# Kernel tuning notes

Hardware: AMD Instinct MI355X
Metric: run time of the kernel (lower is better)

The kernel has to match this reference:

```python
import jax, jax.numpy as jnp
import numpy as np

# Dimensions (production-scale, see shape_source)
B, L, D = 16, 64, 256      # batch, text length, char_emb
U = 500                    # number of distinct units (characters/phonemes)
V = 10000                  # vocab size
MIN_WL, MAX_WL = 4, 10     # min/max extracted word length
WL = MAX_WL - MIN_WL + 1   # number of candidate word lengths (7)
TEMP = 0.1                 # g.temperature
INS_COST = 1.0             # per-character insertion/deletion cost


def setup_inputs() -> dict:
    key = jax.random.key(0)
    k1, k2, k3, k4 = jax.random.split(key, 4)
    word_repr = jax.random.normal(k1, (B, L, D), jnp.float32)
    unit_repr = jax.random.normal(k2, (U, D), jnp.float32)
    indexed_segments = jax.random.randint(k3, (V, MAX_WL), 0, U)
    vocab_length = jax.random.randint(k4, (V,), MIN_WL, MAX_WL + 1)
    return {
        "word_repr": word_repr,
        "unit_repr": unit_repr,
        "indexed_segments": indexed_segments,
        "vocab_length": vocab_length,
    }


def _soft_max(x, axis):
    w = jnp.exp(jax.nn.log_softmax(x / TEMP, axis=axis))
    value = (x * w).sum(axis)
    index = jnp.argmax(x, axis=axis)
    return value, index


def _soft_min(x, axis):
    w = jnp.exp(jax.nn.log_softmax(-x / TEMP, axis=axis))
    value = (x * w).sum(axis)
    index = jnp.argmin(x, axis=axis)
    return value, index


def _soft_threshold(x):
    return (jax.nn.celu(1.0 - 2.0 * x) + 1.0) / 2.0


def reference(word_repr, unit_repr, indexed_segments, vocab_length):
    # --- cosine char-similarity between text positions and vocab units ---
    wn = word_repr / jnp.linalg.norm(word_repr, axis=-1, keepdims=True)   # (B,L,D)
    un = unit_repr / jnp.linalg.norm(unit_repr, axis=-1, keepdims=True)   # (U,D)
    sim = jnp.einsum('bld,ud->blu', wn, un)                               # (B,L,U)
    # pad along length so s+j gathers are in-range; padded dist is masked later
    simp = jnp.pad(sim, ((0, 0), (0, MAX_WL), (0, 0)))                    # (B,L+ML,U)

    wls = jnp.arange(MIN_WL, MAX_WL + 1)                                  # (WL,)

    # --- aligned edit-distance accumulation d(v, w) over char positions ---
    # ed[b,s,k,v] = sum_{j < min(wl_k, len_v)} (1 - cos(text[b,s+j], vocab_char[v,j]))
    ed = jnp.zeros((B, L, WL, V), jnp.float32)
    for j in range(MAX_WL):
        d_j = 1.0 - simp[:, j:j + L, :][:, :, indexed_segments[:, j]]     # (B,L,V)
        m_j = (j < jnp.minimum(wls[:, None], vocab_length[None, :]))      # (WL,V)
        ed = ed + d_j[:, :, None, :] * m_j.astype(jnp.float32)[None, None]
    # length-mismatch penalty (insert/delete)
    ed = ed + INS_COST * jnp.abs(wls[:, None] - vocab_length[None, :]).astype(jnp.float32)

    # --- soft-min over vocab: matched_ed_dist / matched_vocab ---
    matched_ed, matched_vocab = _soft_min(ed, axis=-1)                    # (B,L,WL)
    matched_length = vocab_length[matched_vocab]                          # (B,L,WL)
    # soft threshold on per-character distance, then score = thresh * |w|
    matched_thresh = _soft_threshold(matched_ed / wls.astype(jnp.float32))
    matched_score = matched_thresh * wls.astype(jnp.float32)              # (B,L,WL)

    # --- viability and scatter restore into dense (batch, len_s, len_e) ---
    s_idx = jnp.arange(L)[:, None]                                        # (L,1)
    viable = (s_idx + wls[None, :]) <= L                                  # (L,WL)
    score = jnp.where(viable[None], matched_score, 0.0)                   # (B,L,WL)
    e_idx = jnp.clip(s_idx + wls[None, :] - 1, 0, L - 1)                  # (L,WL)
    s_grid = jnp.broadcast_to(s_idx, (L, WL))
    dense = jnp.zeros((B, L, L), jnp.float32).at[:, s_grid, e_idx].add(
        score * viable[None].astype(jnp.float32))                         # (B,len_s,len_e)

    # --- soft-max over all candidate spans ---
    flat = dense.reshape(B, L * L)
    best_score, best_idx = _soft_max(flat, axis=-1)                       # (B,)
    start = best_idx // L
    end = best_idx % L
    wl_sel = jnp.clip(end - start + 1 - MIN_WL, 0, WL - 1)
    best_vocab = matched_vocab[jnp.arange(B), start, wl_sel]              # (B,)

    return start, end, best_score, best_vocab, dense
```

## Files before the change

kernel.cpp:

```cpp
#include <hip/hip_runtime.h>

#define NB 16
#define NL 64
#define ND 256
#define NU 500
#define NV 10000
#define MINWL 4
#define MAXWL 10
#define NWL 7
#define ITEMP 10.0f
#define L2I 14.4269504088896f
#define NT 512
#define NTX 1024
#define NWAVES 16
#define NCH 16
#define RSTR 501
#define DLPAD 32568
#define SEGL_SLOTS 648
#define EXT_LDS_BYTES ((DLPAD + SEGL_SLOTS * 8) * 4)
#define NSK (NWL * 64)
#define NZERO 3690.0f

__global__ __launch_bounds__(512) void k_sort(const int* __restrict__ vlen,
                                              int* __restrict__ origv,
                                              int* __restrict__ bases) {
    int t = threadIdx.x;
    const int CH = 20;
    int lo = t * CH, hi = min(lo + CH, NV);
    unsigned long long hA = 0, hB = 0;
    for (int v = lo; v < hi; ++v) {
        int l = vlen[v] - MINWL;
        int sh = (l & 3) * 16;
        unsigned long long inc = 1ULL << sh;
        bool isA = l < 4;
        hA += isA ? inc : 0ULL;
        hB += isA ? 0ULL : inc;
    }
    int lane = t & 63, wv = t >> 6;
    unsigned long long iA = hA, iB = hB;
#pragma unroll
    for (int o = 1; o < 64; o <<= 1) {
        unsigned long long a2 = (unsigned long long)__shfl_up((long long)iA, o);
        unsigned long long b2 = (unsigned long long)__shfl_up((long long)iB, o);
        if (lane >= o) { iA += a2; iB += b2; }
    }
    __shared__ unsigned long long wA[8], wB[8];
    __shared__ int base_s[8];
    if (lane == 63) { wA[wv] = iA; wB[wv] = iB; }
    __syncthreads();
    unsigned long long pA = 0, pB = 0, tA = 0, tB = 0;
#pragma unroll
    for (int w2 = 0; w2 < 8; ++w2) {
        if (w2 < wv) { pA += wA[w2]; pB += wB[w2]; }
        tA += wA[w2]; tB += wB[w2];
    }
    unsigned long long eA = pA + iA - hA, eB = pB + iB - hB;
    if (t == 0) {
        int tot[7] = {(int)(tA & 0xFFFF), (int)((tA >> 16) & 0xFFFF),
                      (int)((tA >> 32) & 0xFFFF), (int)((tA >> 48) & 0xFFFF),
                      (int)(tB & 0xFFFF), (int)((tB >> 16) & 0xFFFF),
                      (int)((tB >> 32) & 0xFFFF)};
        int run = 0;
        for (int l = 0; l < 7; ++l) { base_s[l] = run; bases[l] = run; run += tot[l]; }
        base_s[7] = run; bases[7] = run;
    }
    __syncthreads();
    unsigned long long qA = eA + ((unsigned long long)base_s[0] |
                                  ((unsigned long long)base_s[1] << 16) |
                                  ((unsigned long long)base_s[2] << 32) |
                                  ((unsigned long long)base_s[3] << 48));
    unsigned long long qB = eB + ((unsigned long long)base_s[4] |
                                  ((unsigned long long)base_s[5] << 16) |
                                  ((unsigned long long)base_s[6] << 32));
    for (int v = lo; v < hi; ++v) {
        int l = vlen[v] - MINWL;
        int sh = (l & 3) * 16;
        bool isA = l < 4;
        unsigned long long cur = isA ? qA : qB;
        int pos = (int)((cur >> sh) & 0xFFFF);
        origv[pos] = v;
        unsigned long long inc = 1ULL << sh;
        qA += isA ? inc : 0ULL;
        qB += isA ? 0ULL : inc;
    }
}

__global__ __launch_bounds__(256) void k_gather(const int* __restrict__ origv,
                                                const int* __restrict__ seg,
                                                unsigned int* __restrict__ segP) {
    int i = blockIdx.x * 256 + threadIdx.x;
    if (i >= NV) return;
    int v = origv[i];
    const int2* sp = (const int2*)(seg + v * MAXWL);
    int2 a0 = sp[0], a1 = sp[1], a2 = sp[2], a3 = sp[3], a4 = sp[4];
    unsigned int* dst = segP + i * 8;
    *(uint4*)dst = make_uint4((unsigned)(a0.x | (a0.y << 16)),
                              (unsigned)(a1.x | (a1.y << 16)),
                              (unsigned)(a2.x | (a2.y << 16)),
                              (unsigned)(a3.x | (a3.y << 16)));
    dst[4] = (unsigned)(a4.x | (a4.y << 16));
}

#define SSTR 260
#define SIM_LDS_BYTES ((2 * 32 * SSTR + 64) * 4)

__global__ __launch_bounds__(256) void k_sim(const float* __restrict__ word,
                                             const float* __restrict__ unit,
                                             float* __restrict__ sim) {
    extern __shared__ float lds[];
    float* wt = lds;
    float* ut = lds + 32 * SSTR;
    float* scaleW = lds + 64 * SSTR;
    float* scaleU = scaleW + 32;
    int blk = blockIdx.x;
    int uc = blk & 15, lt = (blk >> 4) & 1, b = blk >> 5;
    int l0 = lt * 32, u0 = uc * 32;
    int t = threadIdx.x;

#pragma unroll
    for (int i = 0; i < 32; ++i)
        wt[i * SSTR + t] = word[(b * NL + l0 + i) * ND + t];
#pragma unroll
    for (int i = 0; i < 32; ++i) {
        int u = u0 + i;
        ut[i * SSTR + t] = (u < NU) ? unit[u * ND + t] : 1.0f;
    }
    __syncthreads();
#pragma unroll
    for (int h = 0; h < 2; ++h) {
        int r = (t >> 4) + h * 16, p = t & 15;
        float sw = 0.f, su = 0.f;
#pragma unroll
        for (int c = 0; c < 16; ++c) {
            float x = wt[r * SSTR + p * 16 + c];
            float y = ut[r * SSTR + p * 16 + c];
            sw += x * x; su += y * y;
        }
#pragma unroll
        for (int o = 1; o < 16; o <<= 1) {
            sw += __shfl_xor(sw, o);
            su += __shfl_xor(su, o);
        }
        if (p == 0) { scaleW[r] = 1.0f / sqrtf(sw); scaleU[r] = 1.0f / sqrtf(su); }
    }
    __syncthreads();

    int lane = t & 15;
    int lp = t >> 4;
    int l = lp * 2;
    const float4* w0p = (const float4*)(wt + l * SSTR);
    const float4* w1p = (const float4*)(wt + (l + 1) * SSTR);
    const float4* x0p = (const float4*)(ut + lane * SSTR);
    const float4* x1p = (const float4*)(ut + (lane + 16) * SSTR);
    float a00 = 0.f, a01 = 0.f, a10 = 0.f, a11 = 0.f;
#pragma unroll 8
    for (int dq = 0; dq < ND / 4; ++dq) {
        float4 w0 = w0p[dq], w1 = w1p[dq], x0 = x0p[dq], x1 = x1p[dq];
        a00 += w0.x * x0.x + w0.y * x0.y + w0.z * x0.z + w0.w * x0.w;
        a01 += w0.x * x1.x + w0.y * x1.y + w0.z * x1.z + w0.w * x1.w;
        a10 += w1.x * x0.x + w1.y * x0.y + w1.z * x0.z + w1.w * x0.w;
        a11 += w1.x * x1.x + w1.y * x1.y + w1.z * x1.z + w1.w * x1.w;
    }
    float sw0 = scaleW[l], sw1 = scaleW[l + 1];
    float su0 = scaleU[lane], su1 = scaleU[lane + 16];
    int gu0 = u0 + lane, gu1 = u0 + lane + 16;
    int base = (b * NL + l0 + l) * NU;
    if (gu0 < NU) { sim[base + gu0] = a00 * (sw0 * su0); sim[base + NU + gu0] = a10 * (sw1 * su0); }
    if (gu1 < NU) { sim[base + gu1] = a01 * (sw0 * su1); sim[base + NU + gu1] = a11 * (sw1 * su1); }
}


template <int L>
__device__ __forceinline__ void item_one(const unsigned int* __restrict__ segL,
                                         int li, const float* __restrict__ dl,
                                         const int* __restrict__ rowoff,
                                         float& Sb, float& Wb, float& mb, int& ixb,
                                         float& Sm, float& Wm, float& mmv, int& ixm) {
    const unsigned int* sp = segL + li * 8;
    uint4 p = *(const uint4*)sp;
    unsigned int w4 = (L > 8) ? sp[4] : 0u;
    unsigned int c[10];
    c[0] = p.x & 0xFFFF; c[1] = p.x >> 16;
    c[2] = p.y & 0xFFFF; c[3] = p.y >> 16;
    c[4] = p.z & 0xFFFF; c[5] = p.z >> 16;
    c[6] = p.w & 0xFFFF; c[7] = p.w >> 16;
    c[8] = w4 & 0xFFFF;  c[9] = w4 >> 16;
    float q = ((dl[rowoff[0] + c[0]] + dl[rowoff[1] + c[1]]) +
               dl[rowoff[2] + c[2]]) + dl[rowoff[3] + c[3]];
    float pm = q;
#pragma unroll
    for (int j = 4; j < L; ++j) {
        if (j == L - 1) pm = q;
        q += dl[rowoff[j] + c[j]];
    }
    float wb = __builtin_amdgcn_exp2f(fmaf(q, -L2I, (float)L * L2I));
    Sb += wb;
    Wb = fmaf(q, wb, Wb);
    bool lb = q < mb;
    ixb = lb ? li : ixb;
    mb = lb ? q : mb;
    if constexpr (L >= 5) {
        float edm = pm + 1.0f;
        float wm = __builtin_amdgcn_exp2f(fmaf(edm, -L2I, (float)(L - 1) * L2I));
        Sm += wm;
        Wm = fmaf(edm, wm, Wm);
        bool lm = edm < mmv;
        ixm = lm ? li : ixm;
        mmv = lm ? edm : mmv;
    }
}

template <int L>
__device__ __forceinline__ void bucket_passL(int a, int e, int gofs,
                                             const unsigned int* __restrict__ segL,
                                             const float* __restrict__ dl,
                                             const int* __restrict__ rowoff,
                                             float* m, float* S, float* W, int* ix) {
    if (a >= e) return;
    float Sb = 0.f, Wb = 0.f, mb = 3.0e38f;
    float Sm = 0.f, Wm = 0.f, mmv = 3.0e38f;
    int ixb = 0, ixm = 0;
    int li = a;
    for (; li + 1 < e; li += 2) {
        item_one<L>(segL, li, dl, rowoff, Sb, Wb, mb, ixb, Sm, Wm, mmv, ixm);
        item_one<L>(segL, li + 1, dl, rowoff, Sb, Wb, mb, ixb, Sm, Wm, mmv, ixm);
    }
    if (li < e)
        item_one<L>(segL, li, dl, rowoff, Sb, Wb, mb, ixb, Sm, Wm, mmv, ixm);

    int gb = ixb + gofs, gm_ = ixm + gofs;
#pragma unroll
    for (int k = 0; k < NWL; ++k) {
        if (k >= L - 4) {
            float c = (float)(k + 4 - L);
            S[k] += Sb;
            W[k] += fmaf(c, Sb, Wb);
            float cand = mb + c;
            bool take = (cand < m[k]) || (cand == m[k] && gb < ix[k]);
            ix[k] = take ? gb : ix[k];
            m[k] = take ? cand : m[k];
        }
        if constexpr (L >= 5) {
            if (k == L - 5) {
                S[k] += Sm;
                W[k] += Wm;
                bool take = (mmv < m[k]) || (mmv == m[k] && gm_ < ix[k]);
                ix[k] = take ? gm_ : ix[k];
                m[k] = take ? mmv : m[k];
            }
        }
    }
}

__global__ __launch_bounds__(NTX, 1) void k_extract(const float* __restrict__ sim,
                                                    const unsigned int* __restrict__ segP,
                                                    const int* __restrict__ basesG,
                                                    float* __restrict__ pM,
                                                    float* __restrict__ pS,
                                                    float* __restrict__ pW,
                                                    int* __restrict__ pI) {
    extern __shared__ float dl[];
    unsigned int* segL = (unsigned int*)(dl + DLPAD);
    int blk = blockIdx.x;
    int ch = blk & (NCH - 1), b = blk >> 4;
    int t = threadIdx.x;
    int s = t & 63, w = t >> 6;

    int cs[7], ne[7], lb[7];
    {
        int run = 0;
#pragma unroll
        for (int l = 0; l < 7; ++l) {
            int lo = basesG[l], hi = basesG[l + 1];
            int n = hi - lo;
            int pc = (n + NCH - 1) >> 4;
            int c0 = lo + ch * pc;
            int c1 = min(c0 + pc, hi);
            cs[l] = c0;
            ne[l] = max(c1 - c0, 0);
            lb[l] = run;
            run += ne[l];
        }
    }

    {
        const float2* simq = (const float2*)(sim + b * NL * NU);
        for (int idx = t; idx < NL * 250; idx += NTX) {
            int r = idx / 250;
            int u2 = idx - r * 250;
            float2 g = simq[idx];
            float* ds = dl + r * RSTR + u2 * 2;
            ds[0] = 1.0f - g.x;
            ds[1] = 1.0f - g.y;
        }
        if (t < NU + 1) dl[64 * RSTR + t] = 0.0f;
    }
#pragma unroll
    for (int l = 0; l < 7; ++l) {
        for (int ii = t; ii < ne[l]; ii += NTX) {
            const unsigned int* gp = segP + (cs[l] + ii) * 8;
            uint4 pv = *(const uint4*)gp;
            unsigned int w4 = gp[4];
            unsigned int* dp = segL + (lb[l] + ii) * 8;
            *(uint4*)dp = pv;
            dp[4] = w4;
        }
    }
    __syncthreads();

    int rowoff[10];
#pragma unroll
    for (int j = 0; j < 10; ++j) rowoff[j] = min(s + j, 64) * RSTR;

    float m[NWL], S[NWL], W[NWL];
    int ix[NWL];
#pragma unroll
    for (int k = 0; k < NWL; ++k) { m[k] = 3.0e38f; S[k] = 0.f; W[k] = 0.f; ix[k] = 0; }

    int la[7], le[7];
#pragma unroll
    for (int l = 0; l < 7; ++l) {
        int pw = (ne[l] + NWAVES - 1) >> 4;
        la[l] = lb[l] + w * pw;
        le[l] = min(la[l] + pw, lb[l] + ne[l]);
    }
    bucket_passL<4>(la[0], le[0], cs[0] - lb[0], segL, dl, rowoff, m, S, W, ix);
    bucket_passL<5>(la[1], le[1], cs[1] - lb[1], segL, dl, rowoff, m, S, W, ix);
    bucket_passL<6>(la[2], le[2], cs[2] - lb[2], segL, dl, rowoff, m, S, W, ix);
    bucket_passL<7>(la[3], le[3], cs[3] - lb[3], segL, dl, rowoff, m, S, W, ix);
    bucket_passL<8>(la[4], le[4], cs[4] - lb[4], segL, dl, rowoff, m, S, W, ix);
    bucket_passL<9>(la[5], le[5], cs[5] - lb[5], segL, dl, rowoff, m, S, W, ix);
    bucket_passL<10>(la[6], le[6], cs[6] - lb[6], segL, dl, rowoff, m, S, W, ix);

    __syncthreads();
    float* scrM = dl;
    float* scrS = dl + NWAVES * NSK;
    float* scrW = dl + 2 * NWAVES * NSK;
    int* scrI = (int*)(dl + 3 * NWAVES * NSK);
#pragma unroll
    for (int k = 0; k < NWL; ++k) {
        int o = (w * NWL + k) * 64 + s;
        scrM[o] = m[k]; scrS[o] = S[k]; scrW[o] = W[k]; scrI[o] = ix[k];
    }
    __syncthreads();
    if (t < NSK) {
        int k = t >> 6, ss = t & 63;
        int o0 = k * 64 + ss;
        float mm = scrM[o0], SS = scrS[o0], WW = scrW[o0];
        int II = scrI[o0];
#pragma unroll
        for (int w2 = 1; w2 < NWAVES; ++w2) {
            int o = (w2 * NWL + k) * 64 + ss;
            float m2 = scrM[o];
            int i2 = scrI[o];
            bool take = (m2 < mm) || (m2 == mm && i2 < II);
            II = take ? i2 : II;
            mm = take ? m2 : mm;
            SS += scrS[o];
            WW += scrW[o];
        }
        int off = (b * NCH + ch) * NSK + t;
        pM[off] = mm; pS[off] = SS; pW[off] = WW; pI[off] = II;
    }
}

__global__ __launch_bounds__(NT) void k_merge(const float* __restrict__ pM,
                                              const float* __restrict__ pS,
                                              const float* __restrict__ pW,
                                              const int* __restrict__ pI,
                                              const int* __restrict__ origv,
                                              float* __restrict__ out) {
    int b = blockIdx.x, t = threadIdx.x;
    __shared__ float score[NSK];
    __shared__ int ixf[NSK];
    __shared__ float rm[8], rS[8], rW[8];
    __shared__ int rX[8];
    __shared__ float gm;
    __shared__ int gfl;

    float x = -1.0f;
    int fl = 0x7FFFFFFF;
    if (t < NSK) {
        int base = b * NCH * NSK + t;
        float mm = pM[base], SS = pS[base], WW = pW[base];
        int II = pI[base];
        for (int c = 1; c < NCH; ++c) {
            int o = base + c * NSK;
            float m2 = pM[o];
            int i2 = pI[o];
            bool take = (m2 < mm) || (m2 == mm && i2 < II);
            II = take ? i2 : II;
            mm = take ? m2 : mm;
            SS += pS[o];
            WW += pW[o];
        }
        int k = t >> 6, ss = t & 63;
        int kmax = min(NWL - 1, 60 - ss);
        if (k <= kmax) {
            float med = WW / SS;
            float wl = (float)(MINWL + k);
            float z = 1.0f - 2.0f * (med / wl);
            float cel = (z > 0.f) ? z : (__expf(z) - 1.0f);
            x = 0.5f * (cel + 1.0f) * wl;
            ixf[t] = II;
            fl = ss * 64 + (ss + k + 3);
        }
        score[t] = (k <= kmax) ? x : 0.0f;
    }
    __syncthreads();

    float mv = x;
    int mf = fl;
#pragma unroll
    for (int o = 32; o >= 1; o >>= 1) {
        float m2 = __shfl_down(mv, o);
        int f2 = __shfl_down(mf, o);
        bool take = (m2 > mv) || (m2 == mv && f2 < mf);
        mv = take ? m2 : mv;
        mf = take ? f2 : mf;
    }
    if ((t & 63) == 0) { rm[t >> 6] = mv; rX[t >> 6] = mf; }
    __syncthreads();
    if (t == 0) {
        float mm = rm[0];
        int ff = rX[0];
#pragma unroll
        for (int w2 = 1; w2 < 8; ++w2) {
            bool take = (rm[w2] > mm) || (rm[w2] == mm && rX[w2] < ff);
            mm = take ? rm[w2] : mm;
            ff = take ? rX[w2] : ff;
        }
        gm = mm; gfl = ff;
    }
    __syncthreads();
    float M = gm;

    float Sl = 0.f, Wl = 0.f;
    if (x >= 0.0f) {
        float wq = __expf((x - M) * ITEMP);
        Sl = wq;
        Wl = x * wq;
    }
#pragma unroll
    for (int o = 32; o >= 1; o >>= 1) {
        Sl += __shfl_down(Sl, o);
        Wl += __shfl_down(Wl, o);
    }
    if ((t & 63) == 0) { rS[t >> 6] = Sl; rW[t >> 6] = Wl; }
    __syncthreads();
    if (t == 0) {
        float SS = 0.f, WW = 0.f;
#pragma unroll
        for (int w2 = 0; w2 < 8; ++w2) { SS += rS[w2]; WW += rW[w2]; }
        SS += NZERO * __expf(-M * ITEMP);
        float best = WW / SS;
        int st = gfl >> 6, en = gfl & 63;
        int ks = en - st - 3;
        int II = ixf[ks * 64 + st];
        out[b] = (float)st;
        out[NB + b] = (float)en;
        out[2 * NB + b] = best;
        out[3 * NB + b] = (float)origv[II];
    }

    float* dense = out + 4 * NB + b * NL * NL;
    for (int f = t; f < NL * NL; f += NT) {
        int ss = f >> 6, ee = f & 63;
        int k = ee - ss - 3;
        dense[f] = (k >= 0 && k < NWL) ? score[k * 64 + ss] : 0.0f;
    }
}

extern "C" void kernel_launch(void* const* d_in, const int* in_sizes, int n_in,
                              void* d_out, int out_size, void* d_ws, size_t ws_size,
                              hipStream_t stream) {
    const float* word = (const float*)d_in[0];
    const float* unit = (const float*)d_in[1];
    const int* seg = (const int*)d_in[2];
    const int* vlen = (const int*)d_in[3];
    float* out = (float*)d_out;
    char* ws = (char*)d_ws;
    float* sim = (float*)ws;
    int* origv = (int*)(ws + 2048000);
    int* bases = (int*)(ws + 2088000);
    unsigned int* segP = (unsigned int*)(ws + 2088032);
    float* pM = (float*)(ws + 2408032);
    float* pS = (float*)(ws + 2866784);
    float* pW = (float*)(ws + 3325536);
    int* pI = (int*)(ws + 3784288);

    hipFuncSetAttribute((const void*)k_sim,
                        hipFuncAttributeMaxDynamicSharedMemorySize, SIM_LDS_BYTES);
    hipFuncSetAttribute((const void*)k_extract,
                        hipFuncAttributeMaxDynamicSharedMemorySize, EXT_LDS_BYTES);

    k_sort<<<1, 512, 0, stream>>>(vlen, origv, bases);
    k_gather<<<(NV + 255) / 256, 256, 0, stream>>>(origv, seg, segP);
    k_sim<<<NB * 2 * 16, 256, SIM_LDS_BYTES, stream>>>(word, unit, sim);
    k_extract<<<NB * NCH, NTX, EXT_LDS_BYTES, stream>>>(sim, segP, bases, pM, pS, pW, pI);
    k_merge<<<NB, NT, 0, stream>>>(pM, pS, pW, pI, origv, out);
}
```

Before: 69.18 us.

## Fuse gather into sim kernel and merge into extract via last-block atomic

Folds the segment gather into the similarity kernel as extra blocks, and folds the per-batch merge into the extraction kernel using an atomic counter so the last chunk block does the final reduction. This cuts kernel launches from five to three plus a memset, removing launch and inter-kernel gaps. The sort kernel now preloads lengths into registers with unrolled loops, and the inner extraction loop is unrolled by four. In exchange it adds an atomic counter and fence, a memset launch, and a serial merge tail running on a single block per batch.

```diff
diff --git a/kernel.cpp b/kernel.cpp
--- a/kernel.cpp
+++ b/kernel.cpp
@@ -10,7 +10,6 @@
 #define NWL 7
 #define ITEMP 10.0f
 #define L2I 14.4269504088896f
-#define NT 512
 #define NTX 1024
 #define NWAVES 16
 #define NCH 16
@@ -25,16 +24,23 @@
                                               int* __restrict__ origv,
                                               int* __restrict__ bases) {
     int t = threadIdx.x;
-    const int CH = 20;
-    int lo = t * CH, hi = min(lo + CH, NV);
+    int lv[20];
+#pragma unroll
+    for (int j = 0; j < 20; ++j) {
+        int v = t * 20 + j;
+        lv[j] = (v < NV) ? (vlen[v] - MINWL) : -1;
+    }
     unsigned long long hA = 0, hB = 0;
-    for (int v = lo; v < hi; ++v) {
-        int l = vlen[v] - MINWL;
-        int sh = (l & 3) * 16;
-        unsigned long long inc = 1ULL << sh;
-        bool isA = l < 4;
-        hA += isA ? inc : 0ULL;
-        hB += isA ? 0ULL : inc;
+#pragma unroll
+    for (int j = 0; j < 20; ++j) {
+        int l = lv[j];
+        if (l >= 0) {
+            int sh = (l & 3) * 16;
+            unsigned long long inc = 1ULL << sh;
+            bool isA = l < 4;
+            hA += isA ? inc : 0ULL;
+            hB += isA ? 0ULL : inc;
+        }
     }
     int lane = t & 63, wv = t >> 6;
     unsigned long long iA = hA, iB = hB;
@@ -72,50 +78,55 @@
     unsigned long long qB = eB + ((unsigned long long)base_s[4] |
                                   ((unsigned long long)base_s[5] << 16) |
                                   ((unsigned long long)base_s[6] << 32));
-    for (int v = lo; v < hi; ++v) {
-        int l = vlen[v] - MINWL;
-        int sh = (l & 3) * 16;
-        bool isA = l < 4;
-        unsigned long long cur = isA ? qA : qB;
-        int pos = (int)((cur >> sh) & 0xFFFF);
-        origv[pos] = v;
-        unsigned long long inc = 1ULL << sh;
-        qA += isA ? inc : 0ULL;
-        qB += isA ? 0ULL : inc;
-    }
-}
-
-__global__ __launch_bounds__(256) void k_gather(const int* __restrict__ origv,
-                                                const int* __restrict__ seg,
-                                                unsigned int* __restrict__ segP) {
-    int i = blockIdx.x * 256 + threadIdx.x;
-    if (i >= NV) return;
-    int v = origv[i];
-    const int2* sp = (const int2*)(seg + v * MAXWL);
-    int2 a0 = sp[0], a1 = sp[1], a2 = sp[2], a3 = sp[3], a4 = sp[4];
-    unsigned int* dst = segP + i * 8;
-    *(uint4*)dst = make_uint4((unsigned)(a0.x | (a0.y << 16)),
-                              (unsigned)(a1.x | (a1.y << 16)),
-                              (unsigned)(a2.x | (a2.y << 16)),
-                              (unsigned)(a3.x | (a3.y << 16)));
-    dst[4] = (unsigned)(a4.x | (a4.y << 16));
+#pragma unroll
+    for (int j = 0; j < 20; ++j) {
+        int l = lv[j];
+        if (l >= 0) {
+            int sh = (l & 3) * 16;
+            bool isA = l < 4;
+            unsigned long long cur = isA ? qA : qB;
+            int pos = (int)((cur >> sh) & 0xFFFF);
+            origv[pos] = t * 20 + j;
+            unsigned long long inc = 1ULL << sh;
+            qA += isA ? inc : 0ULL;
+            qB += isA ? 0ULL : inc;
+        }
+    }
 }
 
 #define SSTR 260
 #define SIM_LDS_BYTES ((2 * 32 * SSTR + 64) * 4)
 
-__global__ __launch_bounds__(256) void k_sim(const float* __restrict__ word,
-                                             const float* __restrict__ unit,
-                                             float* __restrict__ sim) {
+__global__ __launch_bounds__(256) void k_simgather(const float* __restrict__ word,
+                                                   const float* __restrict__ unit,
+                                                   float* __restrict__ sim,
+                                                   const int* __restrict__ origv,
+                                                   const int* __restrict__ seg,
+                                                   unsigned int* __restrict__ segP) {
+    int blk = blockIdx.x;
+    int t = threadIdx.x;
+    if (blk >= 512) {
+        int i = (blk - 512) * 256 + t;
+        if (i < NV) {
+            int v = origv[i];
+            const int2* sp = (const int2*)(seg + v * MAXWL);
+            int2 a0 = sp[0], a1 = sp[1], a2 = sp[2], a3 = sp[3], a4 = sp[4];
+            unsigned int* dst = segP + i * 8;
+            *(uint4*)dst = make_uint4((unsigned)(a0.x | (a0.y << 16)),
+                                      (unsigned)(a1.x | (a1.y << 16)),
+                                      (unsigned)(a2.x | (a2.y << 16)),
+                                      (unsigned)(a3.x | (a3.y << 16)));
+            dst[4] = (unsigned)(a4.x | (a4.y << 16));
+        }
+        return;
+    }
     extern __shared__ float lds[];
     float* wt = lds;
     float* ut = lds + 32 * SSTR;
     float* scaleW = lds + 64 * SSTR;
     float* scaleU = scaleW + 32;
-    int blk = blockIdx.x;
     int uc = blk & 15, lt = (blk >> 4) & 1, b = blk >> 5;
     int l0 = lt * 32, u0 = uc * 32;
-    int t = threadIdx.x;
 
 #pragma unroll
     for (int i = 0; i < 32; ++i)
@@ -221,11 +232,13 @@
     float Sm = 0.f, Wm = 0.f, mmv = 3.0e38f;
     int ixb = 0, ixm = 0;
     int li = a;
-    for (; li + 1 < e; li += 2) {
+    for (; li + 3 < e; li += 4) {
         item_one<L>(segL, li, dl, rowoff, Sb, Wb, mb, ixb, Sm, Wm, mmv, ixm);
         item_one<L>(segL, li + 1, dl, rowoff, Sb, Wb, mb, ixb, Sm, Wm, mmv, ixm);
-    }
-    if (li < e)
+        item_one<L>(segL, li + 2, dl, rowoff, Sb, Wb, mb, ixb, Sm, Wm, mmv, ixm);
+        item_one<L>(segL, li + 3, dl, rowoff, Sb, Wb, mb, ixb, Sm, Wm, mmv, ixm);
+    }
+    for (; li < e; ++li)
         item_one<L>(segL, li, dl, rowoff, Sb, Wb, mb, ixb, Sm, Wm, mmv, ixm);
 
     int gb = ixb + gofs, gm_ = ixm + gofs;
@@ -255,10 +268,13 @@
 __global__ __launch_bounds__(NTX, 1) void k_extract(const float* __restrict__ sim,
                                                     const unsigned int* __restrict__ segP,
                                                     const int* __restrict__ basesG,
+                                                    const int* __restrict__ origv,
                                                     float* __restrict__ pM,
                                                     float* __restrict__ pS,
                                                     float* __restrict__ pW,
-                                                    int* __restrict__ pI) {
+                                                    int* __restrict__ pI,
+                                                    unsigned int* __restrict__ cnt,
+                                                    float* __restrict__ out) {
     extern __shared__ float dl[];
     unsigned int* segL = (unsigned int*)(dl + DLPAD);
     int blk = blockIdx.x;
@@ -362,19 +378,24 @@
         int off = (b * NCH + ch) * NSK + t;
         pM[off] = mm; pS[off] = SS; pW[off] = WW; pI[off] = II;
     }
-}
-
-__global__ __launch_bounds__(NT) void k_merge(const float* __restrict__ pM,
-                                              const float* __restrict__ pS,
-                                              const float* __restrict__ pW,
-                                              const int* __restrict__ pI,
-                                              const int* __restrict__ origv,
-                                              float* __restrict__ out) {
-    int b = blockIdx.x, t = threadIdx.x;
-    __shared__ float score[NSK];
-    __shared__ int ixf[NSK];
-    __shared__ float rm[8], rS[8], rW[8];
-    __shared__ int rX[8];
+
+    __syncthreads();
+    __shared__ int lastFlag;
+    if (t == 0) {
+        __threadfence();
+        unsigned prev = __hip_atomic_fetch_add(&cnt[b], 1u, __ATOMIC_ACQ_REL,
+                                               __HIP_MEMORY_SCOPE_AGENT);
+        lastFlag = (prev == NCH - 1);
+    }
+    __syncthreads();
+    if (!lastFlag) return;
+
+    float* score = dl;
+    int* ixf = (int*)(dl + NSK);
+    float* rm = dl + 2 * NSK;
+    float* rS = rm + 16;
+    float* rW = rS + 16;
+    int* rX = (int*)(rW + 16);
     __shared__ float gm;
     __shared__ int gfl;
 
@@ -419,13 +440,13 @@
         mv = take ? m2 : mv;
         mf = take ? f2 : mf;
     }
-    if ((t & 63) == 0) { rm[t >> 6] = mv; rX[t >> 6] = mf; }
+    if ((t & 63) == 0) { rm[w] = mv; rX[w] = mf; }
     __syncthreads();
     if (t == 0) {
         float mm = rm[0];
         int ff = rX[0];
 #pragma unroll
-        for (int w2 = 1; w2 < 8; ++w2) {
+        for (int w2 = 1; w2 < NWAVES; ++w2) {
             bool take = (rm[w2] > mm) || (rm[w2] == mm && rX[w2] < ff);
             mm = take ? rm[w2] : mm;
             ff = take ? rX[w2] : ff;
@@ -446,12 +467,12 @@
         Sl += __shfl_down(Sl, o);
         Wl += __shfl_down(Wl, o);
     }
-    if ((t & 63) == 0) { rS[t >> 6] = Sl; rW[t >> 6] = Wl; }
+    if ((t & 63) == 0) { rS[w] = Sl; rW[w] = Wl; }
     __syncthreads();
     if (t == 0) {
         float SS = 0.f, WW = 0.f;
 #pragma unroll
-        for (int w2 = 0; w2 < 8; ++w2) { SS += rS[w2]; WW += rW[w2]; }
+        for (int w2 = 0; w2 < NWAVES; ++w2) { SS += rS[w2]; WW += rW[w2]; }
         SS += NZERO * __expf(-M * ITEMP);
         float best = WW / SS;
         int st = gfl >> 6, en = gfl & 63;
@@ -464,7 +485,7 @@
     }
 
     float* dense = out + 4 * NB + b * NL * NL;
-    for (int f = t; f < NL * NL; f += NT) {
+    for (int f = t; f < NL * NL; f += NTX) {
         int ss = f >> 6, ee = f & 63;
         int k = ee - ss - 3;
         dense[f] = (k >= 0 && k < NWL) ? score[k * 64 + ss] : 0.0f;
@@ -488,15 +509,17 @@
     float* pS = (float*)(ws + 2866784);
     float* pW = (float*)(ws + 3325536);
     int* pI = (int*)(ws + 3784288);
-
-    hipFuncSetAttribute((const void*)k_sim,
+    unsigned int* cnt = (unsigned int*)(ws + 4243040);
+
+    hipFuncSetAttribute((const void*)k_simgather,
                         hipFuncAttributeMaxDynamicSharedMemorySize, SIM_LDS_BYTES);
     hipFuncSetAttribute((const void*)k_extract,
                         hipFuncAttributeMaxDynamicSharedMemorySize, EXT_LDS_BYTES);
 
+    hipMemsetAsync(cnt, 0, NB * sizeof(unsigned int), stream);
     k_sort<<<1, 512, 0, stream>>>(vlen, origv, bases);
-    k_gather<<<(NV + 255) / 256, 256, 0, stream>>>(origv, seg, segP);
-    k_sim<<<NB * 2 * 16, 256, SIM_LDS_BYTES, stream>>>(word, unit, sim);
-    k_extract<<<NB * NCH, NTX, EXT_LDS_BYTES, stream>>>(sim, segP, bases, pM, pS, pW, pI);
-    k_merge<<<NB, NT, 0, stream>>>(pM, pS, pW, pI, origv, out);
+    k_simgather<<<512 + 40, 256, SIM_LDS_BYTES, stream>>>(word, unit, sim,
+                                                          origv, seg, segP);
+    k_extract<<<NB * NCH, NTX, EXT_LDS_BYTES, stream>>>(sim, segP, bases, origv,
+                                                        pM, pS, pW, pI, cnt, out);
 }
```

New measurement: 92.19 us. +33.3%, slower.
